# Performance work log

Hardware: AMD Instinct MI355X
Metric: run time of the kernel (lower is better)

Reference implementation:

```python
import jax, jax.numpy as jnp
import numpy as np

EPS = 1e-5

def _conv(x, w):
    # 3x3, stride 1, pad 1, NCHW/OIHW
    return jax.lax.conv_general_dilated(x, w, (1, 1), ((1, 1), (1, 1)),
                                        dimension_numbers=('NCHW', 'OIHW', 'NCHW'))

def _bn(x, g, b, m, v):
    inv = jax.lax.rsqrt(v + EPS)
    return (x - m[None, :, None, None]) * (g * inv)[None, :, None, None] + b[None, :, None, None]

def _hardtanh(x):
    return jnp.clip(x, -1.0, 1.0)

def _binarize(x):
    # sign binarization with straight-through estimator (identity gradient)
    s = jnp.where(x >= 0, 1.0, -1.0).astype(x.dtype)
    return x + jax.lax.stop_gradient(s - x)

def _maxpool2(x):
    return jax.lax.reduce_window(x, -jnp.inf, jax.lax.max, (1, 1, 2, 2), (1, 1, 2, 2), 'VALID')

def setup_inputs() -> dict:
    key = jax.random.key(0)
    ks = jax.random.split(key, 8)
    c1, c3, c5 = 128 * 3, 256 * 3, 512 * 3  # infl_ratio = 3
    def W(k, o, i):
        return jax.random.normal(k, (o, i, 3, 3), jnp.float32) * 0.05
    inp = {}
    inp['x'] = jax.random.normal(ks[0], (128, 3, 32, 32), jnp.float32)
    inp['w1'] = W(ks[1], c1, 3)
    inp['w2'] = W(ks[2], c1, c1)
    inp['w3'] = W(ks[3], c3, c1)
    inp['w4'] = W(ks[4], c3, c3)
    inp['w5'] = W(ks[5], c5, c3)
    inp['w6'] = W(ks[6], 512, c5)
    for i, c in zip(range(1, 7), [c1, c1, c3, c3, c5, 512]):
        inp['bn%d_g' % i] = jnp.ones((c,), jnp.float32)
        inp['bn%d_b' % i] = jnp.zeros((c,), jnp.float32)
        inp['bn%d_m' % i] = jnp.zeros((c,), jnp.float32)
        inp['bn%d_v' % i] = jnp.ones((c,), jnp.float32)
    inp['w_lin'] = jax.random.normal(ks[7], (10, 512 * 4 * 4), jnp.float32) * 0.02
    return inp

def reference(x, w1, w2, w3, w4, w5, w6,
              bn1_g, bn1_b, bn1_m, bn1_v,
              bn2_g, bn2_b, bn2_m, bn2_v,
              bn3_g, bn3_b, bn3_m, bn3_v,
              bn4_g, bn4_b, bn4_m, bn4_v,
              bn5_g, bn5_b, bn5_m, bn5_v,
              bn6_g, bn6_b, bn6_m, bn6_v,
              w_lin):
    # block 1: full-precision conv
    h = _hardtanh(_bn(_conv(x, w1), bn1_g, bn1_b, bn1_m, bn1_v))
    # block 2: binarized conv -> maxpool -> BN -> hardtanh
    h = _conv(_binarize(h), _binarize(w2))
    h = _hardtanh(_bn(_maxpool2(h), bn2_g, bn2_b, bn2_m, bn2_v))
    # block 3
    h = _conv(_binarize(h), _binarize(w3))
    h = _hardtanh(_bn(h, bn3_g, bn3_b, bn3_m, bn3_v))
    # block 4
    h = _conv(_binarize(h), _binarize(w4))
    h = _hardtanh(_bn(_maxpool2(h), bn4_g, bn4_b, bn4_m, bn4_v))
    # block 5
    h = _conv(_binarize(h), _binarize(w5))
    h = _hardtanh(_bn(h, bn5_g, bn5_b, bn5_m, bn5_v))
    # block 6
    h = _conv(_binarize(h), _binarize(w6))
    h = _hardtanh(_bn(_maxpool2(h), bn6_g, bn6_b, bn6_m, bn6_v))
    # classifier
    h = h.reshape(-1, 512 * 4 * 4)
    logits = h @ w_lin.T
    return jax.nn.log_softmax(logits, axis=-1)
```

## Files before the change

### kernel.cpp

```cpp
#include <hip/hip_runtime.h>
#include <stdint.h>

#define EPS 1e-5f

typedef __attribute__((ext_vector_type(4))) int i32x4;

__device__ __forceinline__ void gload16(const void* g, void* l)
{
    __builtin_amdgcn_global_load_lds(
        (const __attribute__((address_space(1))) void*)g,
        (__attribute__((address_space(3))) void*)l,
        16, 0, 0);
}

__global__ __launch_bounds__(384) void conv1_a1_kernel(
    const float* __restrict__ x,
    const float* __restrict__ w1,
    const float* __restrict__ g,
    const float* __restrict__ b,
    const float* __restrict__ m,
    const float* __restrict__ v,
    char* __restrict__ a1)
{
    const int bid = blockIdx.x;
    const int n = bid >> 2;
    const int q = bid & 3;
    const int tid = threadIdx.x;

    __shared__ float xin[3][10][34];

    const int y0 = q * 8;
    for (int idx = tid; idx < 3 * 10 * 34; idx += 384) {
        int xx = idx % 34;
        int yy = (idx / 34) % 10;
        int ci = idx / 340;
        int gy = y0 - 1 + yy, gx = xx - 1;
        float val = 0.f;
        if (gy >= 0 && gy < 32 && gx >= 0 && gx < 32)
            val = x[((n * 3 + ci) * 32 + gy) * 32 + gx];
        xin[ci][yy][xx] = val;
    }

    float wr[27];
    {
        const float* wp = w1 + tid * 27;
#pragma unroll
        for (int i = 0; i < 27; ++i) wr[i] = wp[i];
    }
    const float scale = g[tid] * rsqrtf(v[tid] + EPS);
    const float mean = m[tid], beta = b[tid];
    __syncthreads();

    for (int yy = 0; yy < 8; ++yy) {
        const int gy = y0 + yy;
        char* orow = a1 + ((size_t)(n * 34 + gy + 1) * 34 + 1) * 384 + tid;
#pragma unroll
        for (int xp = 0; xp < 32; xp += 2) {
            float a0 = 0.f, a1v = 0.f;
#pragma unroll
            for (int ci = 0; ci < 3; ++ci)
#pragma unroll
                for (int dy = 0; dy < 3; ++dy) {
                    float c0 = xin[ci][yy + dy][xp];
                    float c1 = xin[ci][yy + dy][xp + 1];
                    float c2 = xin[ci][yy + dy][xp + 2];
                    float c3 = xin[ci][yy + dy][xp + 3];
                    const float* wrow = &wr[(ci * 3 + dy) * 3];
                    a0 += c0 * wrow[0] + c1 * wrow[1] + c2 * wrow[2];
                    a1v += c1 * wrow[0] + c2 * wrow[1] + c3 * wrow[2];
                }
            float t0 = (a0 - mean) * scale + beta;
            float t1 = (a1v - mean) * scale + beta;
            orow[(size_t)xp * 384] = (t0 >= 0.f) ? 1 : -1;
            orow[(size_t)(xp + 1) * 384] = (t1 >= 0.f) ? 1 : -1;
        }
    }
}

__global__ void pack_bp_kernel(const float* __restrict__ w,
                               char* __restrict__ bp, int Co, int Ci)
{
    int KC = Ci >> 6;
    int idx = blockIdx.x * 256 + threadIdx.x;
    int total = Co * 9 * Ci;
    if (idx >= total) return;
    int t  = idx & 15;
    int fg = (idx >> 4) & 3;
    int co = (idx >> 6) % Co;
    int s  = idx / (Co * 64);
    int tap = s / KC, kc = s % KC;
    int ci = kc * 64 + fg * 16 + t;
    bp[idx] = (w[((size_t)co * Ci + ci) * 9 + tap] >= 0.f) ? 1 : -1;
}

template<int Ci, int Co, int H, int W, int WM, int GN, int EPI>
__global__ __launch_bounds__(WM * 128, 4) void gemm_async_kernel(
    const char* __restrict__ A,
    const char* __restrict__ Bp,
    const float* __restrict__ g, const float* __restrict__ b,
    const float* __restrict__ m, const float* __restrict__ v,
    char* __restrict__ aout, float* __restrict__ fout)
{
    constexpr int T   = WM * 128;
    constexpr int TM  = WM * 64;
    constexpr int KC  = Ci / 64;
    constexpr int S   = 9 * KC;
    constexpr int WP  = W + 2;
    constexpr int GM  = (128 * H * W) / TM;
    constexpr int BU  = 512 / T;
    constexpr int IPS = 2 + BU;

    __shared__ __align__(16) char lsA[3][TM * 64];
    __shared__ __align__(16) char lsB[3][128 * 64];

    const int id = blockIdx.x;
    const int xcd = id & 7;
    const int s0 = id >> 3;
    const int bm = xcd * (GM / 8) + s0 / GN;
    const int bn = s0 % GN;

    const int tid = threadIdx.x;
    const int lane = tid & 63;
    const int wave = tid >> 6;
    const int wm = wave >> 1, wn = wave & 1;
    const int fr = lane & 15, fg = lane >> 4;

    const char* asrc[2];
    int aoff[2];
#pragma unroll
    for (int q = 0; q < 2; ++q) {
        int unit = wave * 128 + q * 64 + lane;
        int r = unit >> 2, ps = unit & 3;
        int ls = ps ^ ((r >> 1) & 3);
        int gm = bm * TM + r;
        int n_ = gm / (H * W);
        int rr = gm % (H * W);
        int y_ = rr / W, x_ = rr % W;
        asrc[q] = A + ((size_t)(n_ * (H + 2) + y_) * WP + x_) * Ci + ls * 16;
        aoff[q] = wave * 2048 + q * 1024;
    }
    const char* bsrc[BU];
    int boff[BU];
#pragma unroll
    for (int q = 0; q < BU; ++q) {
        int unit = wave * (64 * BU) + q * 64 + lane;
        int col = unit >> 2, ps = unit & 3;
        int ls = ps ^ ((col >> 1) & 3);
        bsrc[q] = Bp + (size_t)bn * 128 * 64 + col * 64 + ls * 16;
        boff[q] = wave * (BU * 1024) + q * 1024;
    }
    const size_t bstep = (size_t)Co * 64;

    auto issue = [&](int sx, int t) {
        int tap = sx / KC, kc = sx % KC;
        int toff = ((tap / 3) * WP + (tap % 3)) * Ci + kc * 64;
#pragma unroll
        for (int q = 0; q < 2; ++q)
            gload16(asrc[q] + toff, &lsA[t][aoff[q]]);
        size_t bo = (size_t)sx * bstep;
#pragma unroll
        for (int q = 0; q < BU; ++q)
            gload16(bsrc[q] + bo, &lsB[t][boff[q]]);
    };

    int raA[4];
#pragma unroll
    for (int i = 0; i < 4; ++i) {
        int row = wm * 64 + i * 16 + fr;
        raA[i] = row * 64 + ((fg ^ ((row >> 1) & 3)) << 4);
    }
    int raB[4];
#pragma unroll
    for (int j = 0; j < 4; ++j) {
        int col = wn * 64 + j * 16 + fr;
        raB[j] = col * 64 + ((fg ^ ((col >> 1) & 3)) << 4);
    }

    i32x4 acc[4][4] = {};

    issue(0, 0);
    issue(1, 1);
    if constexpr (IPS == 3) asm volatile("s_waitcnt vmcnt(3)" ::: "memory");
    else                    asm volatile("s_waitcnt vmcnt(4)" ::: "memory");
    __builtin_amdgcn_sched_barrier(0);
    __builtin_amdgcn_s_barrier();

    int cur = 0;
    for (int s = 0; s < S; ++s) {
        i32x4 af[4], bf[4];
#pragma unroll
        for (int i = 0; i < 4; ++i)
            af[i] = *reinterpret_cast<const i32x4*>(&lsA[cur][raA[i]]);
#pragma unroll
        for (int j = 0; j < 4; ++j)
            bf[j] = *reinterpret_cast<const i32x4*>(&lsB[cur][raB[j]]);

        int sx = (s + 2 < S) ? s + 2 : S - 1;
        int nb = cur + 2; if (nb >= 3) nb -= 3;
        issue(sx, nb);

        __builtin_amdgcn_s_setprio(1);
#pragma unroll
        for (int i = 0; i < 4; ++i)
#pragma unroll
            for (int j = 0; j < 4; ++j)
                acc[i][j] = __builtin_amdgcn_mfma_i32_16x16x64_i8(
                    af[i], bf[j], acc[i][j], 0, 0, 0);
        __builtin_amdgcn_s_setprio(0);

        if constexpr (IPS == 3) asm volatile("s_waitcnt vmcnt(3)" ::: "memory");
        else                    asm volatile("s_waitcnt vmcnt(4)" ::: "memory");
        __builtin_amdgcn_sched_barrier(0);
        __builtin_amdgcn_s_barrier();

        cur = (cur + 1 == 3) ? 0 : cur + 1;
    }

    int colj[4];
    float sc[4], mn[4], bt[4];
#pragma unroll
    for (int j = 0; j < 4; ++j) {
        colj[j] = bn * 128 + wn * 64 + j * 16 + fr;
        sc[j] = g[colj[j]] * rsqrtf(v[colj[j]] + EPS);
        mn[j] = m[colj[j]];
        bt[j] = b[colj[j]];
    }

    if constexpr (EPI == 0) {
        constexpr int HO = H / 2, WO = W / 2;
        const int n = bm >> 2;
        const int Y = 4 * (bm & 3) + wm;
#pragma unroll
        for (int ip = 0; ip < 2; ++ip)
#pragma unroll
            for (int rp = 0; rp < 2; ++rp) {
                int X = ip * 8 + fg * 2 + rp;
#pragma unroll
                for (int j = 0; j < 4; ++j) {
                    int val = max(max(acc[ip][j][2 * rp], acc[ip][j][2 * rp + 1]),
                                  max(acc[ip + 2][j][2 * rp], acc[ip + 2][j][2 * rp + 1]));
                    float t = ((float)val - mn[j]) * sc[j] + bt[j];
                    aout[((size_t)(n * (HO + 2) + Y + 1) * (WO + 2) + X + 1) * Co + colj[j]]
                        = (t >= 0.f) ? 1 : -1;
                }
            }
    } else if constexpr (EPI == 1) {
        const int n = bm;
#pragma unroll
        for (int i = 0; i < 4; ++i) {
            int y = wm * 4 + i;
#pragma unroll
            for (int r = 0; r < 4; ++r) {
                int x = fg * 4 + r;
#pragma unroll
                for (int j = 0; j < 4; ++j) {
                    float t = ((float)acc[i][j][r] - mn[j]) * sc[j] + bt[j];
                    aout[((size_t)(n * (H + 2) + y + 1) * (W + 2) + x + 1) * Co + colj[j]]
                        = (t >= 0.f) ? 1 : -1;
                }
            }
        }
    } else if constexpr (EPI == 2) {
        constexpr int HO = H / 2, WO = W / 2;
        const int n = bm;
#pragma unroll
        for (int iv = 0; iv < 2; ++iv) {
            int Y = wm * 2 + iv;
#pragma unroll
            for (int rp = 0; rp < 2; ++rp) {
                int X = fg * 2 + rp;
#pragma unroll
                for (int j = 0; j < 4; ++j) {
                    int val = max(max(acc[2 * iv][j][2 * rp], acc[2 * iv][j][2 * rp + 1]),
                                  max(acc[2 * iv + 1][j][2 * rp], acc[2 * iv + 1][j][2 * rp + 1]));
                    float t = ((float)val - mn[j]) * sc[j] + bt[j];
                    aout[((size_t)(n * (HO + 2) + Y + 1) * (WO + 2) + X + 1) * Co + colj[j]]
                        = (t >= 0.f) ? 1 : -1;
                }
            }
        }
    } else if constexpr (EPI == 3) {
        const int n = bm * 2 + wm;
#pragma unroll
        for (int i = 0; i < 4; ++i) {
            int y = 2 * i + (fg >> 1);
#pragma unroll
            for (int r = 0; r < 4; ++r) {
                int x = (fg & 1) * 4 + r;
#pragma unroll
                for (int j = 0; j < 4; ++j) {
                    float t = ((float)acc[i][j][r] - mn[j]) * sc[j] + bt[j];
                    aout[((size_t)(n * (H + 2) + y + 1) * (W + 2) + x + 1) * Co + colj[j]]
                        = (t >= 0.f) ? 1 : -1;
                }
            }
        }
    } else {
        const int n = bm * 2 + wm;
#pragma unroll
        for (int i = 0; i < 4; ++i)
#pragma unroll
            for (int rp = 0; rp < 2; ++rp)
#pragma unroll
                for (int j = 0; j < 4; ++j) {
                    int hm = max(acc[i][j][2 * rp], acc[i][j][2 * rp + 1]);
                    int other = __shfl_xor(hm, 32);
                    int val = max(hm, other);
                    if (fg < 2) {
                        int X = (fg & 1) * 2 + rp;
                        float t = ((float)val - mn[j]) * sc[j] + bt[j];
                        t = fminf(1.f, fmaxf(-1.f, t));
                        fout[((size_t)(n * Co + colj[j]) * 4 + i) * 4 + X] = t;
                    }
                }
    }
}

__global__ void classifier_kernel(const float* __restrict__ h,
                                  const float* __restrict__ wl,
                                  float* __restrict__ out)
{
    int n = blockIdx.x;
    int tid = threadIdx.x;
    float acc[10];
#pragma unroll
    for (int j = 0; j < 10; ++j) acc[j] = 0.f;
    for (int k = tid; k < 8192; k += 256) {
        float hv = h[n * 8192 + k];
#pragma unroll
        for (int j = 0; j < 10; ++j) acc[j] += hv * wl[j * 8192 + k];
    }
    __shared__ float sred[256];
    __shared__ float logit[10];
    for (int j = 0; j < 10; ++j) {
        sred[tid] = acc[j];
        __syncthreads();
        for (int s = 128; s > 0; s >>= 1) {
            if (tid < s) sred[tid] += sred[tid + s];
            __syncthreads();
        }
        if (tid == 0) logit[j] = sred[0];
        __syncthreads();
    }
    if (tid == 0) {
        float mx = logit[0];
#pragma unroll
        for (int j = 1; j < 10; ++j) mx = fmaxf(mx, logit[j]);
        float s = 0.f;
#pragma unroll
        for (int j = 0; j < 10; ++j) s += expf(logit[j] - mx);
        float lse = logf(s) + mx;
#pragma unroll
        for (int j = 0; j < 10; ++j) out[n * 10 + j] = logit[j] - lse;
    }
}

extern "C" void kernel_launch(void* const* d_in, const int* in_sizes, int n_in,
                              void* d_out, int out_size, void* d_ws, size_t ws_size,
                              hipStream_t stream)
{
    const float* x    = (const float*)d_in[0];
    const float* w1   = (const float*)d_in[1];
    const float* w2   = (const float*)d_in[2];
    const float* w3   = (const float*)d_in[3];
    const float* w4   = (const float*)d_in[4];
    const float* w5   = (const float*)d_in[5];
    const float* w6   = (const float*)d_in[6];
    const float* bn_g[6], *bn_b[6], *bn_m[6], *bn_v[6];
    for (int i = 0; i < 6; ++i) {
        bn_g[i] = (const float*)d_in[7 + i * 4 + 0];
        bn_b[i] = (const float*)d_in[7 + i * 4 + 1];
        bn_m[i] = (const float*)d_in[7 + i * 4 + 2];
        bn_v[i] = (const float*)d_in[7 + i * 4 + 3];
    }
    const float* wlin = (const float*)d_in[31];
    float* out = (float*)d_out;

    const size_t A1 = (size_t)128 * 34 * 34 * 384;
    const size_t A2 = (size_t)128 * 18 * 18 * 384;
    const size_t A3 = (size_t)128 * 18 * 18 * 768;
    const size_t A4 = (size_t)128 * 10 * 10 * 768;
    const size_t A5 = (size_t)128 * 10 * 10 * 1536;
    const size_t SB = A2;
    const size_t SC = A3;
    const size_t H6 = (size_t)128 * 8192 * 4;

    char* ws = (char*)d_ws;
    auto alloc = [&](size_t bytes) {
        char* p = ws;
        ws += (bytes + 255) & ~(size_t)255;
        return p;
    };
    char*  a1 = (char*)alloc(A1);
    char*  sb = (char*)alloc(SB);
    char*  scs = (char*)alloc(SC);
    float* h6 = (float*)alloc(H6);
    char* bp2 = (char*)alloc((size_t)(9 * 6 + 1) * 384 * 64);
    char* bp3 = (char*)alloc((size_t)(9 * 6 + 1) * 768 * 64);
    char* bp4 = (char*)alloc((size_t)(9 * 12 + 1) * 768 * 64);
    char* bp5 = (char*)alloc((size_t)(9 * 12 + 1) * 1536 * 64);
    char* bp6 = (char*)alloc((size_t)(9 * 24 + 1) * 512 * 64);

    char* a2 = sb;
    char* a3 = scs;
    char* a4 = sb;
    char* a5 = scs;

    {
        int t;
        t = 384 * 9 * 384;
        pack_bp_kernel<<<(t + 255) / 256, 256, 0, stream>>>(w2, bp2, 384, 384);
        t = 768 * 9 * 384;
        pack_bp_kernel<<<(t + 255) / 256, 256, 0, stream>>>(w3, bp3, 768, 384);
        t = 768 * 9 * 768;
        pack_bp_kernel<<<(t + 255) / 256, 256, 0, stream>>>(w4, bp4, 768, 768);
        t = 1536 * 9 * 768;
        pack_bp_kernel<<<(t + 255) / 256, 256, 0, stream>>>(w5, bp5, 1536, 768);
        t = 512 * 9 * 1536;
        pack_bp_kernel<<<(t + 255) / 256, 256, 0, stream>>>(w6, bp6, 512, 1536);
    }

    hipMemsetAsync(a1, 0, A1, stream);
    conv1_a1_kernel<<<128 * 4, 384, 0, stream>>>(
        x, w1, bn_g[0], bn_b[0], bn_m[0], bn_v[0], a1);

    hipMemsetAsync(a2, 0, A2, stream);
    gemm_async_kernel<384, 384, 32, 32, 4, 3, 0>
        <<<512 * 3, 512, 0, stream>>>(a1, bp2, bn_g[1], bn_b[1], bn_m[1], bn_v[1],
                                      a2, nullptr);
    hipMemsetAsync(a3, 0, A3, stream);
    gemm_async_kernel<384, 768, 16, 16, 4, 6, 1>
        <<<128 * 6, 512, 0, stream>>>(a2, bp3, bn_g[2], bn_b[2], bn_m[2], bn_v[2],
                                      a3, nullptr);
    hipMemsetAsync(a4, 0, A4, stream);
    gemm_async_kernel<768, 768, 16, 16, 4, 6, 2>
        <<<128 * 6, 512, 0, stream>>>(a3, bp4, bn_g[3], bn_b[3], bn_m[3], bn_v[3],
                                      a4, nullptr);
    hipMemsetAsync(a5, 0, A5, stream);
    gemm_async_kernel<768, 1536, 8, 8, 2, 12, 3>
        <<<64 * 12, 256, 0, stream>>>(a4, bp5, bn_g[4], bn_b[4], bn_m[4], bn_v[4],
                                      a5, nullptr);
    gemm_async_kernel<1536, 512, 8, 8, 2, 4, 4>
        <<<64 * 4, 256, 0, stream>>>(a5, bp6, bn_g[5], bn_b[5], bn_m[5], bn_v[5],
                                     nullptr, h6);

    classifier_kernel<<<128, 256, 0, stream>>>(h6, wlin, out);
}
```

Measured before the change: 806.7 us.

## Convert binary conv GEMMs to persistent kernels with grid-stride tile loop

The binarized conv GEMM kernel now loops over output tiles with a grid stride instead of mapping one tile per block, and grids are capped at 512 (or 256) blocks. This is meant to cut block launch and tail overhead and keep work resident per CU. The cost is a full vmcnt(0) drain between tiles, so the pipeline restarts its prologue for each tile. With 512 blocks on the 1536-tile layer, the work may also split unevenly, and per-block LDS and occupancy are unchanged.

Result: no change. 798.2 us, median of 3 (-1.0%).

```diff
diff --git a/kernel.cpp b/kernel.cpp
--- a/kernel.cpp
+++ b/kernel.cpp
@@ -94,7 +94,7 @@
 }
 
 template<int Ci, int Co, int H, int W, int WM, int GN, int EPI>
-__global__ __launch_bounds__(WM * 128, 4) void gemm_async_kernel(
+__global__ __launch_bounds__(WM * 128, 4) void gemm_pers_kernel(
     const char* __restrict__ A,
     const char* __restrict__ Bp,
     const float* __restrict__ g, const float* __restrict__ b,
@@ -107,17 +107,12 @@
     constexpr int S   = 9 * KC;
     constexpr int WP  = W + 2;
     constexpr int GM  = (128 * H * W) / TM;
+    constexpr int NT  = GM * GN;
     constexpr int BU  = 512 / T;
     constexpr int IPS = 2 + BU;
 
     __shared__ __align__(16) char lsA[3][TM * 64];
     __shared__ __align__(16) char lsB[3][128 * 64];
-
-    const int id = blockIdx.x;
-    const int xcd = id & 7;
-    const int s0 = id >> 3;
-    const int bm = xcd * (GM / 8) + s0 / GN;
-    const int bn = s0 % GN;
 
     const int tid = threadIdx.x;
     const int lane = tid & 63;
@@ -125,44 +120,6 @@
     const int wm = wave >> 1, wn = wave & 1;
     const int fr = lane & 15, fg = lane >> 4;
 
-    const char* asrc[2];
-    int aoff[2];
-#pragma unroll
-    for (int q = 0; q < 2; ++q) {
-        int unit = wave * 128 + q * 64 + lane;
-        int r = unit >> 2, ps = unit & 3;
-        int ls = ps ^ ((r >> 1) & 3);
-        int gm = bm * TM + r;
-        int n_ = gm / (H * W);
-        int rr = gm % (H * W);
-        int y_ = rr / W, x_ = rr % W;
-        asrc[q] = A + ((size_t)(n_ * (H + 2) + y_) * WP + x_) * Ci + ls * 16;
-        aoff[q] = wave * 2048 + q * 1024;
-    }
-    const char* bsrc[BU];
-    int boff[BU];
-#pragma unroll
-    for (int q = 0; q < BU; ++q) {
-        int unit = wave * (64 * BU) + q * 64 + lane;
-        int col = unit >> 2, ps = unit & 3;
-        int ls = ps ^ ((col >> 1) & 3);
-        bsrc[q] = Bp + (size_t)bn * 128 * 64 + col * 64 + ls * 16;
-        boff[q] = wave * (BU * 1024) + q * 1024;
-    }
-    const size_t bstep = (size_t)Co * 64;
-
-    auto issue = [&](int sx, int t) {
-        int tap = sx / KC, kc = sx % KC;
-        int toff = ((tap / 3) * WP + (tap % 3)) * Ci + kc * 64;
-#pragma unroll
-        for (int q = 0; q < 2; ++q)
-            gload16(asrc[q] + toff, &lsA[t][aoff[q]]);
-        size_t bo = (size_t)sx * bstep;
-#pragma unroll
-        for (int q = 0; q < BU; ++q)
-            gload16(bsrc[q] + bo, &lsB[t][boff[q]]);
-    };
-
     int raA[4];
 #pragma unroll
     for (int i = 0; i < 4; ++i) {
@@ -175,144 +132,199 @@
         int col = wn * 64 + j * 16 + fr;
         raB[j] = col * 64 + ((fg ^ ((col >> 1) & 3)) << 4);
     }
-
-    i32x4 acc[4][4] = {};
-
-    issue(0, 0);
-    issue(1, 1);
-    if constexpr (IPS == 3) asm volatile("s_waitcnt vmcnt(3)" ::: "memory");
-    else                    asm volatile("s_waitcnt vmcnt(4)" ::: "memory");
-    __builtin_amdgcn_sched_barrier(0);
-    __builtin_amdgcn_s_barrier();
-
-    int cur = 0;
-    for (int s = 0; s < S; ++s) {
-        i32x4 af[4], bf[4];
-#pragma unroll
-        for (int i = 0; i < 4; ++i)
-            af[i] = *reinterpret_cast<const i32x4*>(&lsA[cur][raA[i]]);
-#pragma unroll
-        for (int j = 0; j < 4; ++j)
-            bf[j] = *reinterpret_cast<const i32x4*>(&lsB[cur][raB[j]]);
-
-        int sx = (s + 2 < S) ? s + 2 : S - 1;
-        int nb = cur + 2; if (nb >= 3) nb -= 3;
-        issue(sx, nb);
-
-        __builtin_amdgcn_s_setprio(1);
-#pragma unroll
-        for (int i = 0; i < 4; ++i)
-#pragma unroll
-            for (int j = 0; j < 4; ++j)
-                acc[i][j] = __builtin_amdgcn_mfma_i32_16x16x64_i8(
-                    af[i], bf[j], acc[i][j], 0, 0, 0);
-        __builtin_amdgcn_s_setprio(0);
-
+    int aunit_r[2], aunit_ls[2], aoff[2];
+#pragma unroll
+    for (int q = 0; q < 2; ++q) {
+        int unit = wave * 128 + q * 64 + lane;
+        aunit_r[q] = unit >> 2;
+        aunit_ls[q] = (unit & 3) ^ ((aunit_r[q] >> 1) & 3);
+        aoff[q] = wave * 2048 + q * 1024;
+    }
+    int bunit_c[BU], bunit_ls[BU], boff[BU];
+#pragma unroll
+    for (int q = 0; q < BU; ++q) {
+        int unit = wave * (64 * BU) + q * 64 + lane;
+        bunit_c[q] = unit >> 2;
+        bunit_ls[q] = (unit & 3) ^ ((bunit_c[q] >> 1) & 3);
+        boff[q] = wave * (BU * 1024) + q * 1024;
+    }
+    const size_t bstep = (size_t)Co * 64;
+
+    for (int t = blockIdx.x; t < NT; t += gridDim.x) {
+        const int xcd = t & 7;
+        const int s0 = t >> 3;
+        const int bm = xcd * (GM / 8) + s0 / GN;
+        const int bn = s0 % GN;
+
+        const char* asrc[2];
+#pragma unroll
+        for (int q = 0; q < 2; ++q) {
+            int gm = bm * TM + aunit_r[q];
+            int n_ = gm / (H * W);
+            int rr = gm % (H * W);
+            int y_ = rr / W, x_ = rr % W;
+            asrc[q] = A + ((size_t)(n_ * (H + 2) + y_) * WP + x_) * Ci
+                        + aunit_ls[q] * 16;
+        }
+        const char* bsrc[BU];
+#pragma unroll
+        for (int q = 0; q < BU; ++q)
+            bsrc[q] = Bp + (size_t)bn * 128 * 64 + bunit_c[q] * 64
+                         + bunit_ls[q] * 16;
+
+        auto issue = [&](int sx, int tb) {
+            int tap = sx / KC, kc = sx % KC;
+            int toff = ((tap / 3) * WP + (tap % 3)) * Ci + kc * 64;
+#pragma unroll
+            for (int q = 0; q < 2; ++q)
+                gload16(asrc[q] + toff, &lsA[tb][aoff[q]]);
+            size_t bo = (size_t)sx * bstep;
+#pragma unroll
+            for (int q = 0; q < BU; ++q)
+                gload16(bsrc[q] + bo, &lsB[tb][boff[q]]);
+        };
+
+        i32x4 acc[4][4] = {};
+
+        asm volatile("s_waitcnt vmcnt(0)" ::: "memory");
+        __builtin_amdgcn_sched_barrier(0);
+
+        issue(0, 0);
+        issue(1, 1);
         if constexpr (IPS == 3) asm volatile("s_waitcnt vmcnt(3)" ::: "memory");
         else                    asm volatile("s_waitcnt vmcnt(4)" ::: "memory");
         __builtin_amdgcn_sched_barrier(0);
         __builtin_amdgcn_s_barrier();
 
-        cur = (cur + 1 == 3) ? 0 : cur + 1;
-    }
-
-    int colj[4];
-    float sc[4], mn[4], bt[4];
-#pragma unroll
-    for (int j = 0; j < 4; ++j) {
-        colj[j] = bn * 128 + wn * 64 + j * 16 + fr;
-        sc[j] = g[colj[j]] * rsqrtf(v[colj[j]] + EPS);
-        mn[j] = m[colj[j]];
-        bt[j] = b[colj[j]];
-    }
-
-    if constexpr (EPI == 0) {
-        constexpr int HO = H / 2, WO = W / 2;
-        const int n = bm >> 2;
-        const int Y = 4 * (bm & 3) + wm;
-#pragma unroll
-        for (int ip = 0; ip < 2; ++ip)
-#pragma unroll
-            for (int rp = 0; rp < 2; ++rp) {
-                int X = ip * 8 + fg * 2 + rp;
-#pragma unroll
-                for (int j = 0; j < 4; ++j) {
-                    int val = max(max(acc[ip][j][2 * rp], acc[ip][j][2 * rp + 1]),
-                                  max(acc[ip + 2][j][2 * rp], acc[ip + 2][j][2 * rp + 1]));
-                    float t = ((float)val - mn[j]) * sc[j] + bt[j];
-                    aout[((size_t)(n * (HO + 2) + Y + 1) * (WO + 2) + X + 1) * Co + colj[j]]
-                        = (t >= 0.f) ? 1 : -1;
+        int cur = 0;
+        for (int s = 0; s < S; ++s) {
+            i32x4 af[4], bf[4];
+#pragma unroll
+            for (int i = 0; i < 4; ++i)
+                af[i] = *reinterpret_cast<const i32x4*>(&lsA[cur][raA[i]]);
+#pragma unroll
+            for (int j = 0; j < 4; ++j)
+                bf[j] = *reinterpret_cast<const i32x4*>(&lsB[cur][raB[j]]);
+
+            int sx = (s + 2 < S) ? s + 2 : S - 1;
+            int nb = cur + 2; if (nb >= 3) nb -= 3;
+            issue(sx, nb);
+
+            __builtin_amdgcn_s_setprio(1);
+#pragma unroll
+            for (int i = 0; i < 4; ++i)
+#pragma unroll
+                for (int j = 0; j < 4; ++j)
+                    acc[i][j] = __builtin_amdgcn_mfma_i32_16x16x64_i8(
+                        af[i], bf[j], acc[i][j], 0, 0, 0);
+            __builtin_amdgcn_s_setprio(0);
+
+            if constexpr (IPS == 3) asm volatile("s_waitcnt vmcnt(3)" ::: "memory");
+            else                    asm volatile("s_waitcnt vmcnt(4)" ::: "memory");
+            __builtin_amdgcn_sched_barrier(0);
+            __builtin_amdgcn_s_barrier();
+
+            cur = (cur + 1 == 3) ? 0 : cur + 1;
+        }
+
+        int colj[4];
+        float sc[4], mn[4], bt[4];
+#pragma unroll
+        for (int j = 0; j < 4; ++j) {
+            colj[j] = bn * 128 + wn * 64 + j * 16 + fr;
+            sc[j] = g[colj[j]] * rsqrtf(v[colj[j]] + EPS);
+            mn[j] = m[colj[j]];
+            bt[j] = b[colj[j]];
+        }
+
+        if constexpr (EPI == 0) {
+            constexpr int HO = H / 2, WO = W / 2;
+            const int n = bm >> 2;
+            const int Y = 4 * (bm & 3) + wm;
+#pragma unroll
+            for (int ip = 0; ip < 2; ++ip)
+#pragma unroll
+                for (int rp = 0; rp < 2; ++rp) {
+                    int X = ip * 8 + fg * 2 + rp;
+#pragma unroll
+                    for (int j = 0; j < 4; ++j) {
+                        int val = max(max(acc[ip][j][2 * rp], acc[ip][j][2 * rp + 1]),
+                                      max(acc[ip + 2][j][2 * rp], acc[ip + 2][j][2 * rp + 1]));
+                        float tv = ((float)val - mn[j]) * sc[j] + bt[j];
+                        aout[((size_t)(n * (HO + 2) + Y + 1) * (WO + 2) + X + 1) * Co + colj[j]]
+                            = (tv >= 0.f) ? 1 : -1;
+                    }
+                }
+        } else if constexpr (EPI == 1) {
+            const int n = bm;
+#pragma unroll
+            for (int i = 0; i < 4; ++i) {
+                int y = wm * 4 + i;
+#pragma unroll
+                for (int r = 0; r < 4; ++r) {
+                    int x = fg * 4 + r;
+#pragma unroll
+                    for (int j = 0; j < 4; ++j) {
+                        float tv = ((float)acc[i][j][r] - mn[j]) * sc[j] + bt[j];
+                        aout[((size_t)(n * (H + 2) + y + 1) * (W + 2) + x + 1) * Co + colj[j]]
+                            = (tv >= 0.f) ? 1 : -1;
+                    }
                 }
             }
-    } else if constexpr (EPI == 1) {
-        const int n = bm;
-#pragma unroll
-        for (int i = 0; i < 4; ++i) {
-            int y = wm * 4 + i;
-#pragma unroll
-            for (int r = 0; r < 4; ++r) {
-                int x = fg * 4 + r;
-#pragma unroll
-                for (int j = 0; j < 4; ++j) {
-                    float t = ((float)acc[i][j][r] - mn[j]) * sc[j] + bt[j];
-                    aout[((size_t)(n * (H + 2) + y + 1) * (W + 2) + x + 1) * Co + colj[j]]
-                        = (t >= 0.f) ? 1 : -1;
+        } else if constexpr (EPI == 2) {
+            constexpr int HO = H / 2, WO = W / 2;
+            const int n = bm;
+#pragma unroll
+            for (int iv = 0; iv < 2; ++iv) {
+                int Y = wm * 2 + iv;
+#pragma unroll
+                for (int rp = 0; rp < 2; ++rp) {
+                    int X = fg * 2 + rp;
+#pragma unroll
+                    for (int j = 0; j < 4; ++j) {
+                        int val = max(max(acc[2 * iv][j][2 * rp], acc[2 * iv][j][2 * rp + 1]),
+                                      max(acc[2 * iv + 1][j][2 * rp], acc[2 * iv + 1][j][2 * rp + 1]));
+                        float tv = ((float)val - mn[j]) * sc[j] + bt[j];
+                        aout[((size_t)(n * (HO + 2) + Y + 1) * (WO + 2) + X + 1) * Co + colj[j]]
+                            = (tv >= 0.f) ? 1 : -1;
+                    }
                 }
             }
-        }
-    } else if constexpr (EPI == 2) {
-        constexpr int HO = H / 2, WO = W / 2;
-        const int n = bm;
-#pragma unroll
-        for (int iv = 0; iv < 2; ++iv) {
-            int Y = wm * 2 + iv;
-#pragma unroll
-            for (int rp = 0; rp < 2; ++rp) {
-                int X = fg * 2 + rp;
-#pragma unroll
-                for (int j = 0; j < 4; ++j) {
-                    int val = max(max(acc[2 * iv][j][2 * rp], acc[2 * iv][j][2 * rp + 1]),
-                                  max(acc[2 * iv + 1][j][2 * rp], acc[2 * iv + 1][j][2 * rp + 1]));
-                    float t = ((float)val - mn[j]) * sc[j] + bt[j];
-                    aout[((size_t)(n * (HO + 2) + Y + 1) * (WO + 2) + X + 1) * Co + colj[j]]
-                        = (t >= 0.f) ? 1 : -1;
+        } else if constexpr (EPI == 3) {
+            const int n = bm * 2 + wm;
+#pragma unroll
+            for (int i = 0; i < 4; ++i) {
+                int y = 2 * i + (fg >> 1);
+#pragma unroll
+                for (int r = 0; r < 4; ++r) {
+                    int x = (fg & 1) * 4 + r;
+#pragma unroll
+                    for (int j = 0; j < 4; ++j) {
+                        float tv = ((float)acc[i][j][r] - mn[j]) * sc[j] + bt[j];
+                        aout[((size_t)(n * (H + 2) + y + 1) * (W + 2) + x + 1) * Co + colj[j]]
+                            = (tv >= 0.f) ? 1 : -1;
+                    }
                 }
             }
-        }
-    } else if constexpr (EPI == 3) {
-        const int n = bm * 2 + wm;
-#pragma unroll
-        for (int i = 0; i < 4; ++i) {
-            int y = 2 * i + (fg >> 1);
-#pragma unroll
-            for (int r = 0; r < 4; ++r) {
-                int x = (fg & 1) * 4 + r;
-#pragma unroll
-                for (int j = 0; j < 4; ++j) {
-                    float t = ((float)acc[i][j][r] - mn[j]) * sc[j] + bt[j];
-                    aout[((size_t)(n * (H + 2) + y + 1) * (W + 2) + x + 1) * Co + colj[j]]
-                        = (t >= 0.f) ? 1 : -1;
-                }
-            }
-        }
-    } else {
-        const int n = bm * 2 + wm;
-#pragma unroll
-        for (int i = 0; i < 4; ++i)
-#pragma unroll
-            for (int rp = 0; rp < 2; ++rp)
-#pragma unroll
-                for (int j = 0; j < 4; ++j) {
-                    int hm = max(acc[i][j][2 * rp], acc[i][j][2 * rp + 1]);
-                    int other = __shfl_xor(hm, 32);
-                    int val = max(hm, other);
-                    if (fg < 2) {
-                        int X = (fg & 1) * 2 + rp;
-                        float t = ((float)val - mn[j]) * sc[j] + bt[j];
-                        t = fminf(1.f, fmaxf(-1.f, t));
-                        fout[((size_t)(n * Co + colj[j]) * 4 + i) * 4 + X] = t;
+        } else {
+            const int n = bm * 2 + wm;
+#pragma unroll
+            for (int i = 0; i < 4; ++i)
+#pragma unroll
+                for (int rp = 0; rp < 2; ++rp)
+#pragma unroll
+                    for (int j = 0; j < 4; ++j) {
+                        int hm = max(acc[i][j][2 * rp], acc[i][j][2 * rp + 1]);
+                        int other = __shfl_xor(hm, 32);
+                        int val = max(hm, other);
+                        if (fg < 2) {
+                            int X = (fg & 1) * 2 + rp;
+                            float tv = ((float)val - mn[j]) * sc[j] + bt[j];
+                            tv = fminf(1.f, fmaxf(-1.f, tv));
+                            fout[((size_t)(n * Co + colj[j]) * 4 + i) * 4 + X] = tv;
+                        }
                     }
-                }
+        }
     }
 }
 
@@ -379,8 +391,6 @@
     const size_t A1 = (size_t)128 * 34 * 34 * 384;
     const size_t A2 = (size_t)128 * 18 * 18 * 384;
     const size_t A3 = (size_t)128 * 18 * 18 * 768;
-    const size_t A4 = (size_t)128 * 10 * 10 * 768;
-    const size_t A5 = (size_t)128 * 10 * 10 * 1536;
     const size_t SB = A2;
     const size_t SC = A3;
     const size_t H6 = (size_t)128 * 8192 * 4;
@@ -425,24 +435,24 @@
         x, w1, bn_g[0], bn_b[0], bn_m[0], bn_v[0], a1);
 
     hipMemsetAsync(a2, 0, A2, stream);
-    gemm_async_kernel<384, 384, 32, 32, 4, 3, 0>
-        <<<512 * 3, 512, 0, stream>>>(a1, bp2, bn_g[1], bn_b[1], bn_m[1], bn_v[1],
-                                      a2, nullptr);
+    gemm_pers_kernel<384, 384, 32, 32, 4, 3, 0>
+        <<<512, 512, 0, stream>>>(a1, bp2, bn_g[1], bn_b[1], bn_m[1], bn_v[1],
+                                  a2, nullptr);
     hipMemsetAsync(a3, 0, A3, stream);
-    gemm_async_kernel<384, 768, 16, 16, 4, 6, 1>
-        <<<128 * 6, 512, 0, stream>>>(a2, bp3, bn_g[2], bn_b[2], bn_m[2], bn_v[2],
-                                      a3, nullptr);
-    hipMemsetAsync(a4, 0, A4, stream);
-    gemm_async_kernel<768, 768, 16, 16, 4, 6, 2>
-        <<<128 * 6, 512, 0, stream>>>(a3, bp4, bn_g[3], bn_b[3], bn_m[3], bn_v[3],
-                                      a4, nullptr);
-    hipMemsetAsync(a5, 0, A5, stream);
-    gemm_async_kernel<768, 1536, 8, 8, 2, 12, 3>
-        <<<64 * 12, 256, 0, stream>>>(a4, bp5, bn_g[4], bn_b[4], bn_m[4], bn_v[4],
-                                      a5, nullptr);
-    gemm_async_kernel<1536, 512, 8, 8, 2, 4, 4>
-        <<<64 * 4, 256, 0, stream>>>(a5, bp6, bn_g[5], bn_b[5], bn_m[5], bn_v[5],
-                                     nullptr, h6);
+    gemm_pers_kernel<384, 768, 16, 16, 4, 6, 1>
+        <<<512, 512, 0, stream>>>(a2, bp3, bn_g[2], bn_b[2], bn_m[2], bn_v[2],
+                                  a3, nullptr);
+    hipMemsetAsync(a4, 0, (size_t)128 * 10 * 10 * 768, stream);
+    gemm_pers_kernel<768, 768, 16, 16, 4, 6, 2>
+        <<<512, 512, 0, stream>>>(a3, bp4, bn_g[3], bn_b[3], bn_m[3], bn_v[3],
+                                  a4, nullptr);
+    hipMemsetAsync(a5, 0, (size_t)128 * 10 * 10 * 1536, stream);
+    gemm_pers_kernel<768, 1536, 8, 8, 2, 12, 3>
+        <<<512, 256, 0, stream>>>(a4, bp5, bn_g[4], bn_b[4], bn_m[4], bn_v[4],
+                                  a5, nullptr);
+    gemm_pers_kernel<1536, 512, 8, 8, 2, 4, 4>
+        <<<256, 256, 0, stream>>>(a5, bp6, bn_g[5], bn_b[5], bn_m[5], bn_v[5],
+                                  nullptr, h6);
 
     classifier_kernel<<<128, 256, 0, stream>>>(h6, wlin, out);
 }
```
